# Kernel tuning notes

Hardware: AMD Instinct MI355X
Metric: run time of the kernel (lower is better)

Reference implementation:

```python
import jax, jax.numpy as jnp
import numpy as np

# BEV grid constants from init_kwargs (gen_dx_bx)
DX = jnp.array([0.3, 0.3, 20.0], dtype=jnp.float32)          # dx
BX_LO = jnp.array([-54.0, -54.0, -10.0], dtype=jnp.float32)  # bx - dx/2 = lower bound
NXX, NXY, NZ = 360, 360, 1                                    # nx = (360, 360, 1)


def setup_inputs() -> dict:
    key = jax.random.key(0)
    k1, k2, k3 = jax.random.split(key, 3)
    B, D, fH, fW, C = 4, 118, 32, 88, 80
    iH, iW = 256, 704
    x = jax.random.normal(k1, (B, D, fH, fW, C), dtype=jnp.float32)
    # frustum exactly as create_frustum(): (D, fH, fW, 3) with (u, v, depth)
    ds = jnp.arange(1.0, 60.0, 0.5, dtype=jnp.float32)[:, None, None] * jnp.ones((1, fH, fW), jnp.float32)
    xs = jnp.linspace(0.0, iW - 1.0, fW, dtype=jnp.float32)[None, None, :] * jnp.ones((D, fH, 1), jnp.float32)
    ys = jnp.linspace(0.0, iH - 1.0, fH, dtype=jnp.float32)[None, :, None] * jnp.ones((D, 1, fW), jnp.float32)
    frustum = jnp.stack([xs, ys, ds], axis=-1)
    # realistic pinhole intrinsics (well-conditioned for torch.inverse analog)
    fx = 560.0
    K = jnp.array([[fx, 0.0, (iW - 1) / 2.0], [0.0, fx, (iH - 1) / 2.0], [0.0, 0.0, 1.0]], dtype=jnp.float32)
    intrins = jnp.tile(K[None], (B, 1, 1))
    # camera->lidar: cam z -> lidar x, cam x -> -y, cam y -> -z, with small yaw jitter per sample
    Rbase = jnp.array([[0.0, 0.0, 1.0], [-1.0, 0.0, 0.0], [0.0, -1.0, 0.0]], dtype=jnp.float32)
    ang = jax.random.uniform(k2, (B,), minval=-0.2, maxval=0.2, dtype=jnp.float32)
    c, s = jnp.cos(ang), jnp.sin(ang)
    z0, o = jnp.zeros_like(c), jnp.ones_like(c)
    Ryaw = jnp.stack([jnp.stack([c, -s, z0], -1), jnp.stack([s, c, z0], -1), jnp.stack([z0, z0, o], -1)], axis=-2)
    rots = Ryaw @ Rbase[None]
    trans = jax.random.normal(k3, (B, 3), dtype=jnp.float32) * 0.5
    return {"x": x, "camera2lidar_rots": rots, "camera2lidar_trans": trans, "intrins": intrins, "frustum": frustum}


def reference(x, camera2lidar_rots, camera2lidar_trans, intrins, frustum):
    B, D, H, W, C = x.shape
    # --- get_geometry ---
    # unproject pixel (u,v,d) -> camera coords (u*d, v*d, d)
    pts = jnp.concatenate([frustum[..., :2] * frustum[..., 2:3], frustum[..., 2:3]], axis=-1)  # (D,H,W,3)
    combine = camera2lidar_rots @ jnp.linalg.inv(intrins)  # (B,3,3)
    geom = jnp.einsum('bij,dhwj->bdhwi', combine, pts) + camera2lidar_trans[:, None, None, None, :]  # (B,D,H,W,3)
    # --- bev_pool ---
    feats = x.reshape(-1, C)                                      # (Nprime, C)
    # torch .long() truncates toward zero -> numpy-style astype cast matches
    coords = ((geom - BX_LO) / DX).astype(jnp.int32).reshape(-1, 3)  # (Nprime, 3) voxel ix
    Np = feats.shape[0]
    batch_ix = jnp.repeat(jnp.arange(B, dtype=jnp.int32), Np // B)
    nx = jnp.array([NXX, NXY, NZ], dtype=jnp.int32)
    kept = jnp.all((coords >= 0) & (coords < nx), axis=-1)
    # linear voxel index ordered (b, z, x, y); out-of-range points go to a trash segment
    lin = ((batch_ix * NZ + coords[:, 2]) * NXX + coords[:, 0]) * NXY + coords[:, 1]
    nseg = B * NZ * NXX * NXY
    lin = jnp.where(kept, lin, nseg)
    pooled = jax.ops.segment_sum(feats, lin, num_segments=nseg + 1)[:-1]  # (B*Z*X*Y, C)
    out = pooled.reshape(B, NZ, NXX, NXY, C).transpose(0, 1, 4, 2, 3)     # (B, Z, C, X, Y)
    # torch: cat(unbind(dim=2 of (B,C,Z,X,Y)), dim=1) == (B, Z*C, X, Y) with Z-major blocks
    final = out.reshape(B, NZ * C, NXX, NXY)
    return final
```

## Files before the change

### kernel.cpp

```cpp
#include <hip/hip_runtime.h>
#include <hip/hip_bf16.h>

constexpr int B  = 4;
constexpr int D  = 118;
constexpr int FH = 32;
constexpr int FW = 88;
constexpr int C  = 80;
constexpr int NX = 360, NY = 360;
constexpr int XY = NX * NY;
constexpr int OUT_PER_B = C * XY;
constexpr int WPB = 16;
constexpr int NWB = (FW + WPB - 1) / WPB;
constexpr int THREADS = WPB * (C / 4);


__global__ __launch_bounds__(THREADS)
void bev_rayreduce_kernel(const float* __restrict__ x,
                          const float* __restrict__ rots,
                          const float* __restrict__ trans,
                          const float* __restrict__ intr,
                          const float* __restrict__ fr,
                          float* __restrict__ out) {
    const int g  = blockIdx.x;
    const int wg = g % NWB;
    const int bd = g / NWB;
    const int d  = bd % D;
    const int b  = bd / D;

    const int tid = threadIdx.x;
    const int wl  = tid / 20;
    const int q   = tid - wl * 20;
    const int w   = wg * WPB + wl;
    const bool active = (w < FW);

    const float* K = intr + b * 9;
    const float* R = rots + b * 9;
    const float i00 = 1.0f / K[0];
    const float i11 = 1.0f / K[4];
    const float i22 = 1.0f / K[8];
    const float i12 = -(K[5] * i22) / K[4];
    const float i01 = -(K[1] * i11) / K[0];
    const float i02 = -(fmaf(K[1], i12, K[2] * i22)) / K[0];
    const float inv[9] = { i00, i01, i02, 0.f, i11, i12, 0.f, 0.f, i22 };
    float cb[9];
    #pragma unroll
    for (int i = 0; i < 3; ++i) {
        #pragma unroll
        for (int j = 0; j < 3; ++j) {
            float a = R[i * 3 + 0] * inv[0 * 3 + j];
            a = fmaf(R[i * 3 + 1], inv[1 * 3 + j], a);
            a = fmaf(R[i * 3 + 2], inv[2 * 3 + j], a);
            cb[i * 3 + j] = a;
        }
    }
    const float tx = trans[b * 3 + 0];
    const float ty = trans[b * 3 + 1];
    const float tz = trans[b * 3 + 2];

    const float* frd = fr + (size_t)d * FH * FW * 3;
    const float dd = frd[2];
    const float u  = active ? frd[w * 3 + 0] : 0.f;
    const float v0 = frd[1];

    const float p0 = u * dd;
    const float p2 = dd;
    const float p1_0 = v0 * dd;

    const float g0 = fmaf(cb[2], p2, fmaf(cb[1], p1_0, cb[0] * p0)) + tx;
    const float g1 = fmaf(cb[5], p2, fmaf(cb[4], p1_0, cb[3] * p0)) + ty;
    const int c0 = (int)((g0 + 54.0f) / 0.3f);
    const int c1 = (int)((g1 + 54.0f) / 0.3f);
    const bool inXY = active && c0 >= 0 && c0 < NX && c1 >= 0 && c1 < NY;

    unsigned zmask = 0;
    #pragma unroll
    for (int h = 0; h < FH; ++h) {
        const float vh = frd[h * FW * 3 + 1];
        const float p1h = vh * dd;
        const float g2 = fmaf(cb[8], p2, fmaf(cb[7], p1h, cb[6] * p0)) + tz;
        const int c2 = (int)((g2 + 10.0f) / 20.0f);
        if (c2 == 0) zmask |= (1u << h);
    }

    if (inXY && zmask) {
        float4 acc = make_float4(0.f, 0.f, 0.f, 0.f);
        const float* xb = x + (((size_t)b * D + d) * FH) * (FW * C)
                            + (size_t)w * C + q * 4;
        #pragma unroll
        for (int h = 0; h < FH; ++h) {
            if ((zmask >> h) & 1u) {
                const float4 v = *(const float4*)(xb + (size_t)h * (FW * C));
                acc.x += v.x; acc.y += v.y; acc.z += v.z; acc.w += v.w;
            }
        }
        float* o = out + (size_t)b * OUT_PER_B + (size_t)(q * 4) * XY
                       + c0 * NY + c1;
        unsafeAtomicAdd(o,          acc.x);
        unsafeAtomicAdd(o + XY,     acc.y);
        unsafeAtomicAdd(o + 2 * XY, acc.z);
        unsafeAtomicAdd(o + 3 * XY, acc.w);
    }
}

extern "C" void kernel_launch(void* const* d_in, const int* in_sizes, int n_in,
                              void* d_out, int out_size, void* d_ws, size_t ws_size,
                              hipStream_t stream) {
    const float* x     = (const float*)d_in[0];
    const float* rots  = (const float*)d_in[1];
    const float* trans = (const float*)d_in[2];
    const float* intr  = (const float*)d_in[3];
    const float* fr    = (const float*)d_in[4];
    float* out = (float*)d_out;

    hipMemsetAsync(d_out, 0, (size_t)out_size * sizeof(float), stream);

    const int nblocks = B * D * NWB;
    bev_rayreduce_kernel<<<nblocks, THREADS, 0, stream>>>(x, rots, trans, intr, fr, out);
}
```

Baseline: 667.0 us.

## Replace scatter atomics with per-cell ray buckets and a gather kernel

The ray-reduce kernel now writes per-ray pooled features to a workspace buffer. It also appends each ray id to a fixed-capacity (64) bucket per BEV cell, using an atomic counter. A second kernel walks each cell's bucket, sums the ray features and writes every output element directly, which replaces the full-output memset and the float atomics. The bucket cap can drop rays if more than 64 land in one cell, and the per-ray workspace adds extra memory traffic.

```diff
diff --git a/kernel.cpp b/kernel.cpp
--- a/kernel.cpp
+++ b/kernel.cpp
@@ -9,80 +9,111 @@
 constexpr int NX = 360, NY = 360;
 constexpr int XY = NX * NY;
 constexpr int OUT_PER_B = C * XY;
+constexpr int CELLS = B * XY;
+constexpr int RPB = D * FW;
+constexpr int CAP = 64;
+
 constexpr int WPB = 16;
 constexpr int NWB = (FW + WPB - 1) / WPB;
-constexpr int THREADS = WPB * (C / 4);
+constexpr int K1_THREADS = WPB * (C / 4);
+
+constexpr size_t CNT_BYTES    = (size_t)CELLS * 4;
+constexpr size_t BUCKET_BYTES = (size_t)CELLS * CAP * 2;
+constexpr size_t RAYFEAT_OFF  = CNT_BYTES + BUCKET_BYTES;
 
 
-__global__ __launch_bounds__(THREADS)
-void bev_rayreduce_kernel(const float* __restrict__ x,
-                          const float* __restrict__ rots,
-                          const float* __restrict__ trans,
-                          const float* __restrict__ intr,
-                          const float* __restrict__ fr,
-                          float* __restrict__ out) {
+__global__ __launch_bounds__(K1_THREADS)
+void ray_reduce_kernel(const float* __restrict__ x,
+                       const float* __restrict__ rots,
+                       const float* __restrict__ trans,
+                       const float* __restrict__ intr,
+                       const float* __restrict__ fr,
+                       int* __restrict__ cnt,
+                       unsigned short* __restrict__ bucket,
+                       float* __restrict__ rayfeat) {
     const int g  = blockIdx.x;
     const int wg = g % NWB;
     const int bd = g / NWB;
     const int d  = bd % D;
     const int b  = bd / D;
 
+    __shared__ int      sCell[WPB];
+    __shared__ unsigned sMask[WPB];
+
     const int tid = threadIdx.x;
-    const int wl  = tid / 20;
-    const int q   = tid - wl * 20;
-    const int w   = wg * WPB + wl;
-    const bool active = (w < FW);
 
-    const float* K = intr + b * 9;
-    const float* R = rots + b * 9;
-    const float i00 = 1.0f / K[0];
-    const float i11 = 1.0f / K[4];
-    const float i22 = 1.0f / K[8];
-    const float i12 = -(K[5] * i22) / K[4];
-    const float i01 = -(K[1] * i11) / K[0];
-    const float i02 = -(fmaf(K[1], i12, K[2] * i22)) / K[0];
-    const float inv[9] = { i00, i01, i02, 0.f, i11, i12, 0.f, 0.f, i22 };
-    float cb[9];
-    #pragma unroll
-    for (int i = 0; i < 3; ++i) {
-        #pragma unroll
-        for (int j = 0; j < 3; ++j) {
-            float a = R[i * 3 + 0] * inv[0 * 3 + j];
-            a = fmaf(R[i * 3 + 1], inv[1 * 3 + j], a);
-            a = fmaf(R[i * 3 + 2], inv[2 * 3 + j], a);
-            cb[i * 3 + j] = a;
+    if (tid < WPB) {
+        const int w = wg * WPB + tid;
+        int cell = -1;
+        unsigned zmask = 0;
+        if (w < FW) {
+            const float* K = intr + b * 9;
+            const float* R = rots + b * 9;
+            const float i00 = 1.0f / K[0];
+            const float i11 = 1.0f / K[4];
+            const float i22 = 1.0f / K[8];
+            const float i12 = -(K[5] * i22) / K[4];
+            const float i01 = -(K[1] * i11) / K[0];
+            const float i02 = -(fmaf(K[1], i12, K[2] * i22)) / K[0];
+            const float inv[9] = { i00, i01, i02, 0.f, i11, i12, 0.f, 0.f, i22 };
+            float cb[9];
+            #pragma unroll
+            for (int i = 0; i < 3; ++i) {
+                #pragma unroll
+                for (int j = 0; j < 3; ++j) {
+                    float a = R[i * 3 + 0] * inv[0 * 3 + j];
+                    a = fmaf(R[i * 3 + 1], inv[1 * 3 + j], a);
+                    a = fmaf(R[i * 3 + 2], inv[2 * 3 + j], a);
+                    cb[i * 3 + j] = a;
+                }
+            }
+            const float tx = trans[b * 3 + 0];
+            const float ty = trans[b * 3 + 1];
+            const float tz = trans[b * 3 + 2];
+
+            const float* frd = fr + (size_t)d * FH * FW * 3;
+            const float dd = frd[2];
+            const float u  = frd[w * 3 + 0];
+            const float v0 = frd[1];
+
+            const float p0 = u * dd;
+            const float p2 = dd;
+            const float p1_0 = v0 * dd;
+
+            const float g0 = fmaf(cb[2], p2, fmaf(cb[1], p1_0, cb[0] * p0)) + tx;
+            const float g1 = fmaf(cb[5], p2, fmaf(cb[4], p1_0, cb[3] * p0)) + ty;
+            const int c0 = (int)((g0 + 54.0f) / 0.3f);
+            const int c1 = (int)((g1 + 54.0f) / 0.3f);
+
+            #pragma unroll
+            for (int h = 0; h < FH; ++h) {
+                const float vh = frd[h * FW * 3 + 1];
+                const float p1h = vh * dd;
+                const float g2 = fmaf(cb[8], p2, fmaf(cb[7], p1h, cb[6] * p0)) + tz;
+                const int c2 = (int)((g2 + 10.0f) / 20.0f);
+                if (c2 == 0) zmask |= (1u << h);
+            }
+
+            if (c0 >= 0 && c0 < NX && c1 >= 0 && c1 < NY && zmask != 0) {
+                cell = b * XY + c0 * NY + c1;
+            }
+        }
+        sCell[tid] = cell;
+        sMask[tid] = zmask;
+        if (cell >= 0) {
+            const int rid = d * FW + w;
+            const int idx = atomicAdd(&cnt[cell], 1);
+            if (idx < CAP) bucket[(size_t)cell * CAP + idx] = (unsigned short)rid;
         }
     }
-    const float tx = trans[b * 3 + 0];
-    const float ty = trans[b * 3 + 1];
-    const float tz = trans[b * 3 + 2];
+    __syncthreads();
 
-    const float* frd = fr + (size_t)d * FH * FW * 3;
-    const float dd = frd[2];
-    const float u  = active ? frd[w * 3 + 0] : 0.f;
-    const float v0 = frd[1];
-
-    const float p0 = u * dd;
-    const float p2 = dd;
-    const float p1_0 = v0 * dd;
-
-    const float g0 = fmaf(cb[2], p2, fmaf(cb[1], p1_0, cb[0] * p0)) + tx;
-    const float g1 = fmaf(cb[5], p2, fmaf(cb[4], p1_0, cb[3] * p0)) + ty;
-    const int c0 = (int)((g0 + 54.0f) / 0.3f);
-    const int c1 = (int)((g1 + 54.0f) / 0.3f);
-    const bool inXY = active && c0 >= 0 && c0 < NX && c1 >= 0 && c1 < NY;
-
-    unsigned zmask = 0;
-    #pragma unroll
-    for (int h = 0; h < FH; ++h) {
-        const float vh = frd[h * FW * 3 + 1];
-        const float p1h = vh * dd;
-        const float g2 = fmaf(cb[8], p2, fmaf(cb[7], p1h, cb[6] * p0)) + tz;
-        const int c2 = (int)((g2 + 10.0f) / 20.0f);
-        if (c2 == 0) zmask |= (1u << h);
-    }
-
-    if (inXY && zmask) {
+    const int wl = tid / 20;
+    const int q  = tid - wl * 20;
+    const int w  = wg * WPB + wl;
+    const int cell = sCell[wl];
+    if (cell >= 0) {
+        const unsigned zmask = sMask[wl];
         float4 acc = make_float4(0.f, 0.f, 0.f, 0.f);
         const float* xb = x + (((size_t)b * D + d) * FH) * (FW * C)
                             + (size_t)w * C + q * 4;
@@ -93,12 +124,46 @@
                 acc.x += v.x; acc.y += v.y; acc.z += v.z; acc.w += v.w;
             }
         }
-        float* o = out + (size_t)b * OUT_PER_B + (size_t)(q * 4) * XY
-                       + c0 * NY + c1;
-        unsafeAtomicAdd(o,          acc.x);
-        unsafeAtomicAdd(o + XY,     acc.y);
-        unsafeAtomicAdd(o + 2 * XY, acc.z);
-        unsafeAtomicAdd(o + 3 * XY, acc.w);
+        const size_t gray = (size_t)b * RPB + d * FW + w;
+        *(float4*)(rayfeat + gray * C + q * 4) = acc;
+    }
+}
+
+constexpr int GTH = 256;
+
+__global__ __launch_bounds__(GTH)
+void gather_kernel(const int* __restrict__ cnt,
+                   const unsigned short* __restrict__ bucket,
+                   const float* __restrict__ rayfeat,
+                   float* __restrict__ out) {
+    const int b    = blockIdx.y;
+    const int flat = blockIdx.x * GTH + threadIdx.x;
+    if (flat >= XY) return;
+    const int cell = b * XY + flat;
+    const int n = min(cnt[cell], CAP);
+    const unsigned short* bk = bucket + (size_t)cell * CAP;
+    float* ob = out + (size_t)b * OUT_PER_B + flat;
+
+    #pragma unroll
+    for (int ch = 0; ch < 4; ++ch) {
+        float acc[20];
+        #pragma unroll
+        for (int j = 0; j < 20; ++j) acc[j] = 0.f;
+        for (int i = 0; i < n; ++i) {
+            const float* rf = rayfeat + ((size_t)b * RPB + bk[i]) * C + ch * 20;
+            #pragma unroll
+            for (int j5 = 0; j5 < 5; ++j5) {
+                const float4 v = *(const float4*)(rf + j5 * 4);
+                acc[j5 * 4 + 0] += v.x;
+                acc[j5 * 4 + 1] += v.y;
+                acc[j5 * 4 + 2] += v.z;
+                acc[j5 * 4 + 3] += v.w;
+            }
+        }
+        #pragma unroll
+        for (int j = 0; j < 20; ++j) {
+            ob[(size_t)(ch * 20 + j) * XY] = acc[j];
+        }
     }
 }
 
@@ -112,8 +177,15 @@
     const float* fr    = (const float*)d_in[4];
     float* out = (float*)d_out;
 
-    hipMemsetAsync(d_out, 0, (size_t)out_size * sizeof(float), stream);
+    int* cnt               = (int*)d_ws;
+    unsigned short* bucket = (unsigned short*)((char*)d_ws + CNT_BYTES);
+    float* rayfeat         = (float*)((char*)d_ws + RAYFEAT_OFF);
 
-    const int nblocks = B * D * NWB;
-    bev_rayreduce_kernel<<<nblocks, THREADS, 0, stream>>>(x, rots, trans, intr, fr, out);
+    hipMemsetAsync(cnt, 0, CNT_BYTES, stream);
+
+    ray_reduce_kernel<<<B * D * NWB, K1_THREADS, 0, stream>>>(
+        x, rots, trans, intr, fr, cnt, bucket, rayfeat);
+
+    dim3 ggrid((XY + GTH - 1) / GTH, B);
+    gather_kernel<<<ggrid, GTH, 0, stream>>>(cnt, bucket, rayfeat, out);
 }
```

New measurement: 664.5 us. Within noise of the previous version (-0.4%).
